# Optimization experiments

Hardware: AMD Instinct MI355X
Metric: run time of the kernel (lower is better)

Reference implementation:

```python
import jax, jax.numpy as jnp
import numpy as np

N = 100000
E = 1600000
D_IN = 64
D_OUT = 64
LN_EPS = 1e-5


def setup_inputs() -> dict:
    key = jax.random.key(0)
    k1, k2, k3 = jax.random.split(key, 3)
    x = jax.random.normal(k1, (N, D_IN), dtype=jnp.float32)
    edge_index = jax.random.randint(k2, (2, E), 0, N, dtype=jnp.int64)
    # nn.Linear(in_dim*2, out_dim): weight [out, 2*in], bias [out]
    W = jax.random.normal(k3, (D_OUT, 2 * D_IN), dtype=jnp.float32) * (1.0 / np.sqrt(2 * D_IN))
    b = jnp.zeros((D_OUT,), dtype=jnp.float32)
    gamma = jnp.ones((D_OUT,), dtype=jnp.float32)
    beta = jnp.zeros((D_OUT,), dtype=jnp.float32)
    return {"x": x, "edge_index": edge_index, "W": W, "b": b, "gamma": gamma, "beta": beta}


def reference(x, edge_index, W, b, gamma, beta):
    i, j = edge_index[0], edge_index[1]          # dst, src
    msg = x[j]                                    # [E, D] gather of source features
    agg = jax.ops.segment_sum(msg, i, num_segments=N)                      # [N, D]
    deg = jax.ops.segment_sum(jnp.ones((E,), x.dtype), i, num_segments=N)  # [N]
    agg = agg / jnp.maximum(deg, 1.0)[:, None]    # mean aggregation
    h = jnp.concatenate([x, agg], axis=-1)        # [N, 2D]
    out = jax.nn.relu(h @ W.T + b)                # [N, D_OUT]
    # LayerNorm over last dim (dropout p=0 -> identity)
    mu = jnp.mean(out, axis=-1, keepdims=True)
    var = jnp.var(out, axis=-1, keepdims=True)
    return (out - mu) * jax.lax.rsqrt(var + LN_EPS) * gamma + beta
```

## Files before the change

kernel.cpp:

```cpp
#include <hip/hip_runtime.h>

#define LN_EPS 1e-5f
#define SBSH   14
#define NSB    7
#define CAP1   268288
#define CPS    131
#define BN     128
#define BC     2368
#define NBK    782
#define CSTRIDE 8

typedef __attribute__((ext_vector_type(8))) short short8;
typedef __attribute__((ext_vector_type(8))) unsigned short ushort8;
typedef __attribute__((ext_vector_type(4))) float v4f;

__device__ __forceinline__ unsigned short f2bf(float f) {
    union { float f; unsigned u; } v; v.f = f;
    unsigned r = (v.u + 0x7fffu + ((v.u >> 16) & 1u)) >> 16;
    return (unsigned short)r;
}
__device__ __forceinline__ float bf2f(unsigned short h) {
    union { unsigned u; float f; } v; v.u = ((unsigned)h) << 16;
    return v.f;
}

__global__ __launch_bounds__(256) void bin1_kernel(
    const int* __restrict__ ei, int* __restrict__ cursor1,
    int* __restrict__ pairs1, const float* __restrict__ W,
    unsigned short* __restrict__ WTB, const float4* __restrict__ x4,
    ushort4* __restrict__ xb4, int E, int N)
{
    __shared__ int h[64];
    __shared__ int hbase[64];
    int t = threadIdx.x;
    int cp = t & 7;

    if (blockIdx.x == 0) {
        for (int i = t; i < 8192; i += 256) {
            int j = i & 7, l = (i >> 3) & 63, st = i >> 9;
            int s = st >> 2, tt = st & 3;
            WTB[i] = f2bf(W[(tt * 16 + (l & 15)) * 128 + s * 32 + (l >> 4) * 8 + j]);
        }
    }
    {
        int total4 = N * 16;
        for (int i = blockIdx.x * 256 + t; i < total4; i += gridDim.x * 256) {
            float4 v = x4[i];
            ushort4 u;
            u.x = f2bf(v.x); u.y = f2bf(v.y); u.z = f2bf(v.z); u.w = f2bf(v.w);
            xb4[i] = u;
        }
    }

    for (int i = t; i < 64; i += 256) h[i] = 0;
    __syncthreads();
    int e0 = blockIdx.x * 4096;
    int dstA[16], srcA[16], rkA[16];
    #pragma unroll
    for (int i = 0; i < 16; ++i) {
        int e = e0 + i * 256 + t;
        int dst = 0, src = 0, rk = -1;
        if (e < E) {
            dst = ei[e]; src = ei[E + e];
            if ((unsigned)dst < (unsigned)N) {
                rk = atomicAdd(&h[cp * 8 + (dst >> SBSH)], 1);
                if ((unsigned)src >= (unsigned)N) src = 0;
            } else { dst = 0; }
        }
        dstA[i] = dst; srcA[i] = src; rkA[i] = rk;
    }
    __syncthreads();
    if (t < 8) {
        int tot = 0;
        #pragma unroll
        for (int c = 0; c < 8; ++c) tot += h[c * 8 + t];
        int gb = tot ? atomicAdd(&cursor1[t * 16], tot) : 0;
        int run = gb;
        #pragma unroll
        for (int c = 0; c < 8; ++c) { hbase[c * 8 + t] = run; run += h[c * 8 + t]; }
    }
    __syncthreads();
    #pragma unroll
    for (int i = 0; i < 16; ++i) {
        if (rkA[i] >= 0) {
            int sb = dstA[i] >> SBSH;
            int slot = hbase[cp * 8 + sb] + rkA[i];
            if (slot < CAP1)
                pairs1[(size_t)sb * CAP1 + slot] = ((dstA[i] & 16383) << 17) | srcA[i];
        }
    }
}

__global__ __launch_bounds__(256) void bin2_kernel(
    const int* __restrict__ cursor1, const int* __restrict__ pairs1,
    int* __restrict__ cursor2, int* __restrict__ pairs2)
{
    __shared__ int h[128], hbase[128];
    int t = threadIdx.x;
    int sb = blockIdx.x / CPS;
    int off0 = (blockIdx.x % CPS) * 2048;
    int tot = cursor1[sb * 16]; if (tot > CAP1) tot = CAP1;
    int m = tot - off0;
    if (m <= 0) return;
    if (m > 2048) m = 2048;
    if (t < 128) h[t] = 0;
    __syncthreads();
    const int* p1 = pairs1 + (size_t)sb * CAP1 + off0;
    int pvA[8], rkA[8];
    #pragma unroll
    for (int i = 0; i < 8; ++i) {
        int idx = i * 256 + t;
        int pv = 0, rk = -1;
        if (idx < m) { pv = p1[idx]; rk = atomicAdd(&h[(pv >> 24) & 127], 1); }
        pvA[i] = pv; rkA[i] = rk;
    }
    __syncthreads();
    if (t < 128) {
        int c = h[t];
        hbase[t] = c ? atomicAdd(&cursor2[(sb * 128 + t) * CSTRIDE], c) : 0;
    }
    __syncthreads();
    #pragma unroll
    for (int i = 0; i < 8; ++i) {
        if (rkA[i] >= 0) {
            int bl = (pvA[i] >> 24) & 127;
            int g = sb * 128 + bl;
            int slot = hbase[bl] + rkA[i];
            if (g < NBK && slot < BC)
                pairs2[(size_t)g * BC + slot] = pvA[i] & 0xFFFFFF;
        }
    }
}

__global__ __launch_bounds__(1024) void sortgather_kernel(
    const int* __restrict__ cursor2, const int* __restrict__ pairs2,
    const unsigned short* __restrict__ xb, unsigned short* __restrict__ aggb, int N)
{
    __shared__ int srcS[BC];
    __shared__ int cnt[BN], off[BN], cur[BN];
    int t = threadIdx.x;
    int g = blockIdx.x;
    int bsize = cursor2[g * CSTRIDE]; if (bsize > BC) bsize = BC;
    const int* pb = pairs2 + (size_t)g * BC;

    if (t < BN) cnt[t] = 0;
    __syncthreads();
    for (int i = t; i < bsize; i += 1024) atomicAdd(&cnt[(pb[i] >> 17) & 127], 1);
    __syncthreads();
    if (t < BN) off[t] = cnt[t];
    __syncthreads();
    for (int s = 1; s < BN; s <<= 1) {
        int v = (t < BN && t >= s) ? off[t - s] : 0;
        __syncthreads();
        if (t < BN) off[t] += v;
        __syncthreads();
    }
    if (t < BN) { int ex = off[t] - cnt[t]; off[t] = ex; cur[t] = ex; }
    __syncthreads();
    for (int i = t; i < bsize; i += 1024) {
        int p = pb[i];
        int pos = atomicAdd(&cur[(p >> 17) & 127], 1);
        srcS[pos] = p & 0x1FFFF;
    }
    __syncthreads();

    int lane = t & 63, wv = t >> 6;
    int g8 = lane >> 3, f8 = lane & 7;
    int ln = wv * 8 + g8;
    int deg = cnt[ln], base = off[ln];

    float acc[8];
    #pragma unroll
    for (int k = 0; k < 8; ++k) acc[k] = 0.f;

    int j = 0;
    for (; j + 2 <= deg; j += 2) {
        int s0 = srcS[base + j];
        int s1 = srcS[base + j + 1];
        short8 a0 = *(const short8*)(xb + (size_t)s0 * 64 + f8 * 8);
        short8 a1 = *(const short8*)(xb + (size_t)s1 * 64 + f8 * 8);
        #pragma unroll
        for (int k = 0; k < 8; ++k) acc[k] += bf2f((unsigned short)a0[k]);
        #pragma unroll
        for (int k = 0; k < 8; ++k) acc[k] += bf2f((unsigned short)a1[k]);
    }
    if (j < deg) {
        int s0 = srcS[base + j];
        short8 a0 = *(const short8*)(xb + (size_t)s0 * 64 + f8 * 8);
        #pragma unroll
        for (int k = 0; k < 8; ++k) acc[k] += bf2f((unsigned short)a0[k]);
    }

    int node = g * BN + ln;
    if (node < N) {
        float inv = 1.0f / fmaxf((float)deg, 1.0f);
        ushort8 r;
        #pragma unroll
        for (int k = 0; k < 8; ++k) r[k] = f2bf(acc[k] * inv);
        *(ushort8*)(aggb + (size_t)node * 64 + f8 * 8) = r;
    }
}

__global__ __launch_bounds__(256) void linear_kernel(
    const unsigned short* __restrict__ xb, const unsigned short* __restrict__ aggb,
    const unsigned short* __restrict__ WTB, const float* __restrict__ b,
    const float* __restrict__ gamma, const float* __restrict__ beta,
    float* __restrict__ out, int N)
{
    int lane = threadIdx.x & 63;
    int wv   = threadIdx.x >> 6;
    int nb   = blockIdx.x * 64 + wv * 16;
    if (nb >= N) return;
    int c = lane & 15, q = lane >> 4;
    int nm = nb + c; if (nm >= N) nm = N - 1;

    short8 bf[4][4];
    const short8* WB = (const short8*)WTB;
    #pragma unroll
    for (int s = 0; s < 4; ++s)
        #pragma unroll
        for (int tt = 0; tt < 4; ++tt)
            bf[s][tt] = WB[(s * 4 + tt) * 64 + lane];

    v4f acc[4];
    #pragma unroll
    for (int tt = 0; tt < 4; ++tt) acc[tt] = 0.f;

    #pragma unroll
    for (int s = 0; s < 2; ++s) {
        short8 af = *(const short8*)(xb + (size_t)nm * 64 + s * 32 + q * 8);
        #pragma unroll
        for (int tt = 0; tt < 4; ++tt)
            acc[tt] = __builtin_amdgcn_mfma_f32_16x16x32_bf16(af, bf[s][tt], acc[tt], 0, 0, 0);
    }
    #pragma unroll
    for (int s = 0; s < 2; ++s) {
        short8 af = *(const short8*)(aggb + (size_t)nm * 64 + s * 32 + q * 8);
        #pragma unroll
        for (int tt = 0; tt < 4; ++tt)
            acc[tt] = __builtin_amdgcn_mfma_f32_16x16x32_bf16(af, bf[2 + s][tt], acc[tt], 0, 0, 0);
    }

    float bb[4], gg[4], be[4];
    #pragma unroll
    for (int tt = 0; tt < 4; ++tt) {
        bb[tt] = b[tt * 16 + c];
        gg[tt] = gamma[tt * 16 + c];
        be[tt] = beta[tt * 16 + c];
    }
    #pragma unroll
    for (int r = 0; r < 4; ++r) {
        int node = nb + q * 4 + r;
        float v[4]; float s0 = 0.f, q0 = 0.f;
        #pragma unroll
        for (int tt = 0; tt < 4; ++tt) {
            float vv = acc[tt][r] + bb[tt];
            vv = fmaxf(vv, 0.f);
            v[tt] = vv; s0 += vv; q0 += vv * vv;
        }
        #pragma unroll
        for (int o = 1; o <= 8; o <<= 1) {
            s0 += __shfl_xor(s0, o);
            q0 += __shfl_xor(q0, o);
        }
        float mu  = s0 * (1.0f / 64.0f);
        float var = q0 * (1.0f / 64.0f) - mu * mu;
        float rs  = rsqrtf(var + LN_EPS);
        if (node < N) {
            #pragma unroll
            for (int tt = 0; tt < 4; ++tt)
                out[(size_t)node * 64 + tt * 16 + c] = (v[tt] - mu) * rs * gg[tt] + be[tt];
        }
    }
}

extern "C" void kernel_launch(void* const* d_in, const int* in_sizes, int n_in,
                              void* d_out, int out_size, void* d_ws, size_t ws_size,
                              hipStream_t stream)
{
    const float* x     = (const float*)d_in[0];
    const int*   ei    = (const int*)d_in[1];
    const float* W     = (const float*)d_in[2];
    const float* b     = (const float*)d_in[3];
    const float* gamma = (const float*)d_in[4];
    const float* beta  = (const float*)d_in[5];

    int N = in_sizes[0] / 64;
    int E = in_sizes[1] / 2;

    int* wsI = (int*)d_ws;
    int* cursor1 = wsI;
    int* cursor2 = wsI + 128;
    unsigned short* WTB = (unsigned short*)(wsI + 128 + 896 * CSTRIDE);
    int* pairs2 = wsI + 128 + 896 * CSTRIDE + 4096;
    unsigned short* xb = (unsigned short*)(pairs2 + (size_t)NBK * BC);

    int* pairs1 = (int*)d_out;
    unsigned short* aggb = (unsigned short*)d_in[1];

    float* out = (float*)d_out;

    hipMemsetAsync(cursor1, 0, (size_t)(128 + 896 * CSTRIDE) * sizeof(int), stream);

    int b1 = (E + 4095) / 4096;
    bin1_kernel<<<b1, 256, 0, stream>>>(ei, cursor1, pairs1, W, WTB,
                                        (const float4*)x, (ushort4*)xb, E, N);

    bin2_kernel<<<NSB * CPS, 256, 0, stream>>>(cursor1, pairs1, cursor2, pairs2);

    sortgather_kernel<<<NBK, 1024, 0, stream>>>(cursor2, pairs2, xb, aggb, N);

    int lb = (N + 63) / 64;
    linear_kernel<<<lb, 256, 0, stream>>>(xb, aggb, WTB, b, gamma, beta, out, N);
}
```

Measured before the change: 172.1 us.

## Gather from feature-sliced bf16 copy of x to improve gather cache locality

The bf16 conversion pass also writes a second copy of x split into four 16-feature slices, each laid out contiguously across nodes. The aggregation kernel then makes four passes, one per slice, with 4-byte per-lane loads, so each pass touches a 3.2 MB working set that fits in cache better than the full 12.8 MB table. The cost is an extra 12.8 MB write in the first kernel, re-reading the source indices four times, and narrower per-lane loads.

Result: slower. 201.5 us (+17.1%).

```diff
diff --git a/kernel.cpp b/kernel.cpp
--- a/kernel.cpp
+++ b/kernel.cpp
@@ -23,12 +23,18 @@
     union { unsigned u; float f; } v; v.u = ((unsigned)h) << 16;
     return v.f;
 }
+__device__ __forceinline__ float bflo(unsigned v) {
+    union { unsigned u; float f; } w; w.u = v << 16; return w.f;
+}
+__device__ __forceinline__ float bfhi(unsigned v) {
+    union { unsigned u; float f; } w; w.u = v & 0xFFFF0000u; return w.f;
+}
 
 __global__ __launch_bounds__(256) void bin1_kernel(
     const int* __restrict__ ei, int* __restrict__ cursor1,
     int* __restrict__ pairs1, const float* __restrict__ W,
     unsigned short* __restrict__ WTB, const float4* __restrict__ x4,
-    ushort4* __restrict__ xb4, int E, int N)
+    ushort4* __restrict__ xb4, ushort4* __restrict__ xs4, int E, int N)
 {
     __shared__ int h[64];
     __shared__ int hbase[64];
@@ -49,6 +55,8 @@
             ushort4 u;
             u.x = f2bf(v.x); u.y = f2bf(v.y); u.z = f2bf(v.z); u.w = f2bf(v.w);
             xb4[i] = u;
+            int node = i >> 4, c = i & 15;
+            xs4[(((c >> 2) * N + node) << 2) + (c & 3)] = u;
         }
     }
 
@@ -134,7 +142,7 @@
 
 __global__ __launch_bounds__(1024) void sortgather_kernel(
     const int* __restrict__ cursor2, const int* __restrict__ pairs2,
-    const unsigned short* __restrict__ xb, unsigned short* __restrict__ aggb, int N)
+    const unsigned short* __restrict__ xs, unsigned short* __restrict__ aggb, int N)
 {
     __shared__ int srcS[BC];
     __shared__ int cnt[BN], off[BN], cur[BN];
@@ -168,36 +176,39 @@
     int g8 = lane >> 3, f8 = lane & 7;
     int ln = wv * 8 + g8;
     int deg = cnt[ln], base = off[ln];
-
-    float acc[8];
-    #pragma unroll
-    for (int k = 0; k < 8; ++k) acc[k] = 0.f;
-
-    int j = 0;
-    for (; j + 2 <= deg; j += 2) {
-        int s0 = srcS[base + j];
-        int s1 = srcS[base + j + 1];
-        short8 a0 = *(const short8*)(xb + (size_t)s0 * 64 + f8 * 8);
-        short8 a1 = *(const short8*)(xb + (size_t)s1 * 64 + f8 * 8);
-        #pragma unroll
-        for (int k = 0; k < 8; ++k) acc[k] += bf2f((unsigned short)a0[k]);
-        #pragma unroll
-        for (int k = 0; k < 8; ++k) acc[k] += bf2f((unsigned short)a1[k]);
-    }
-    if (j < deg) {
-        int s0 = srcS[base + j];
-        short8 a0 = *(const short8*)(xb + (size_t)s0 * 64 + f8 * 8);
-        #pragma unroll
-        for (int k = 0; k < 8; ++k) acc[k] += bf2f((unsigned short)a0[k]);
-    }
-
     int node = g * BN + ln;
-    if (node < N) {
-        float inv = 1.0f / fmaxf((float)deg, 1.0f);
-        ushort8 r;
-        #pragma unroll
-        for (int k = 0; k < 8; ++k) r[k] = f2bf(acc[k] * inv);
-        *(ushort8*)(aggb + (size_t)node * 64 + f8 * 8) = r;
+    float inv = 1.0f / fmaxf((float)deg, 1.0f);
+
+    const unsigned* xs32 = (const unsigned*)xs;
+
+    #pragma unroll
+    for (int p = 0; p < 4; ++p) {
+        size_t pbase = (size_t)p * N * 8;
+        float a0 = 0.f, a1 = 0.f;
+        int j = 0;
+        for (; j + 4 <= deg; j += 4) {
+            int s0 = srcS[base + j];
+            int s1 = srcS[base + j + 1];
+            int s2 = srcS[base + j + 2];
+            int s3 = srcS[base + j + 3];
+            unsigned v0 = xs32[pbase + (size_t)s0 * 8 + f8];
+            unsigned v1 = xs32[pbase + (size_t)s1 * 8 + f8];
+            unsigned v2 = xs32[pbase + (size_t)s2 * 8 + f8];
+            unsigned v3 = xs32[pbase + (size_t)s3 * 8 + f8];
+            a0 += bflo(v0); a1 += bfhi(v0);
+            a0 += bflo(v1); a1 += bfhi(v1);
+            a0 += bflo(v2); a1 += bfhi(v2);
+            a0 += bflo(v3); a1 += bfhi(v3);
+        }
+        for (; j < deg; ++j) {
+            int s0 = srcS[base + j];
+            unsigned v0 = xs32[pbase + (size_t)s0 * 8 + f8];
+            a0 += bflo(v0); a1 += bfhi(v0);
+        }
+        if (node < N) {
+            unsigned pk = (unsigned)f2bf(a0 * inv) | ((unsigned)f2bf(a1 * inv) << 16);
+            *(unsigned*)(aggb + (size_t)node * 64 + p * 16 + f8 * 2) = pk;
+        }
     }
 }
 
@@ -294,6 +305,7 @@
     unsigned short* WTB = (unsigned short*)(wsI + 128 + 896 * CSTRIDE);
     int* pairs2 = wsI + 128 + 896 * CSTRIDE + 4096;
     unsigned short* xb = (unsigned short*)(pairs2 + (size_t)NBK * BC);
+    unsigned short* xs = xb + (size_t)N * 64;
 
     int* pairs1 = (int*)d_out;
     unsigned short* aggb = (unsigned short*)d_in[1];
@@ -304,11 +316,11 @@
 
     int b1 = (E + 4095) / 4096;
     bin1_kernel<<<b1, 256, 0, stream>>>(ei, cursor1, pairs1, W, WTB,
-                                        (const float4*)x, (ushort4*)xb, E, N);
+                                        (const float4*)x, (ushort4*)xb, (ushort4*)xs, E, N);
 
     bin2_kernel<<<NSB * CPS, 256, 0, stream>>>(cursor1, pairs1, cursor2, pairs2);
 
-    sortgather_kernel<<<NBK, 1024, 0, stream>>>(cursor2, pairs2, xb, aggb, N);
+    sortgather_kernel<<<NBK, 1024, 0, stream>>>(cursor2, pairs2, xs, aggb, N);
 
     int lb = (N + 63) / 64;
     linear_kernel<<<lb, 256, 0, stream>>>(xb, aggb, WTB, b, gamma, beta, out, N);
```

## Fuse linear+LayerNorm into sortgather kernel via LDS-staged aggregates

Applied to the files above, without the earlier changes.

Removes the separate linear_kernel launch by keeping each block's 128 aggregated node rows in padded shared memory and running the MFMA linear, ReLU and LayerNorm in the first 8 waves of the same block. This avoids writing aggb to global memory and reading it back, and saves one launch. In exchange, only 8 of the 16 waves do the epilogue, so they run serially after the gather phase. The added LDS buffer may also lower occupancy, and the launch_bounds hint of 8 may push register pressure.

New measurement: 167.5 us. -2.7%, faster.

```diff
diff --git a/kernel.cpp b/kernel.cpp
--- a/kernel.cpp
+++ b/kernel.cpp
@@ -9,6 +9,7 @@
 #define BC     2368
 #define NBK    782
 #define CSTRIDE 8
+#define ASTR   72
 
 typedef __attribute__((ext_vector_type(8))) short short8;
 typedef __attribute__((ext_vector_type(8))) unsigned short ushort8;
@@ -132,12 +133,15 @@
     }
 }
 
-__global__ __launch_bounds__(1024) void sortgather_kernel(
+__global__ __launch_bounds__(1024, 8) void sortgather_kernel(
     const int* __restrict__ cursor2, const int* __restrict__ pairs2,
-    const unsigned short* __restrict__ xb, unsigned short* __restrict__ aggb, int N)
+    const unsigned short* __restrict__ xb, const unsigned short* __restrict__ WTB,
+    const float* __restrict__ b, const float* __restrict__ gamma,
+    const float* __restrict__ beta, float* __restrict__ out, int N)
 {
     __shared__ int srcS[BC];
     __shared__ int cnt[BN], off[BN], cur[BN];
+    __shared__ __align__(16) unsigned short aggS[BN * ASTR];
     int t = threadIdx.x;
     int g = blockIdx.x;
     int bsize = cursor2[g * CSTRIDE]; if (bsize > BC) bsize = BC;
@@ -191,85 +195,73 @@
         for (int k = 0; k < 8; ++k) acc[k] += bf2f((unsigned short)a0[k]);
     }
 
-    int node = g * BN + ln;
-    if (node < N) {
+    {
         float inv = 1.0f / fmaxf((float)deg, 1.0f);
         ushort8 r;
         #pragma unroll
         for (int k = 0; k < 8; ++k) r[k] = f2bf(acc[k] * inv);
-        *(ushort8*)(aggb + (size_t)node * 64 + f8 * 8) = r;
-    }
-}
-
-__global__ __launch_bounds__(256) void linear_kernel(
-    const unsigned short* __restrict__ xb, const unsigned short* __restrict__ aggb,
-    const unsigned short* __restrict__ WTB, const float* __restrict__ b,
-    const float* __restrict__ gamma, const float* __restrict__ beta,
-    float* __restrict__ out, int N)
-{
-    int lane = threadIdx.x & 63;
-    int wv   = threadIdx.x >> 6;
-    int nb   = blockIdx.x * 64 + wv * 16;
-    if (nb >= N) return;
-    int c = lane & 15, q = lane >> 4;
-    int nm = nb + c; if (nm >= N) nm = N - 1;
-
-    short8 bf[4][4];
-    const short8* WB = (const short8*)WTB;
-    #pragma unroll
-    for (int s = 0; s < 4; ++s)
-        #pragma unroll
-        for (int tt = 0; tt < 4; ++tt)
-            bf[s][tt] = WB[(s * 4 + tt) * 64 + lane];
-
-    v4f acc[4];
-    #pragma unroll
-    for (int tt = 0; tt < 4; ++tt) acc[tt] = 0.f;
-
-    #pragma unroll
-    for (int s = 0; s < 2; ++s) {
-        short8 af = *(const short8*)(xb + (size_t)nm * 64 + s * 32 + q * 8);
-        #pragma unroll
-        for (int tt = 0; tt < 4; ++tt)
-            acc[tt] = __builtin_amdgcn_mfma_f32_16x16x32_bf16(af, bf[s][tt], acc[tt], 0, 0, 0);
-    }
-    #pragma unroll
-    for (int s = 0; s < 2; ++s) {
-        short8 af = *(const short8*)(aggb + (size_t)nm * 64 + s * 32 + q * 8);
-        #pragma unroll
-        for (int tt = 0; tt < 4; ++tt)
-            acc[tt] = __builtin_amdgcn_mfma_f32_16x16x32_bf16(af, bf[2 + s][tt], acc[tt], 0, 0, 0);
-    }
-
-    float bb[4], gg[4], be[4];
-    #pragma unroll
-    for (int tt = 0; tt < 4; ++tt) {
-        bb[tt] = b[tt * 16 + c];
-        gg[tt] = gamma[tt * 16 + c];
-        be[tt] = beta[tt * 16 + c];
-    }
-    #pragma unroll
-    for (int r = 0; r < 4; ++r) {
-        int node = nb + q * 4 + r;
-        float v[4]; float s0 = 0.f, q0 = 0.f;
-        #pragma unroll
-        for (int tt = 0; tt < 4; ++tt) {
-            float vv = acc[tt][r] + bb[tt];
-            vv = fmaxf(vv, 0.f);
-            v[tt] = vv; s0 += vv; q0 += vv * vv;
-        }
-        #pragma unroll
-        for (int o = 1; o <= 8; o <<= 1) {
-            s0 += __shfl_xor(s0, o);
-            q0 += __shfl_xor(q0, o);
-        }
-        float mu  = s0 * (1.0f / 64.0f);
-        float var = q0 * (1.0f / 64.0f) - mu * mu;
-        float rs  = rsqrtf(var + LN_EPS);
-        if (node < N) {
+        *(ushort8*)(aggS + ln * ASTR + f8 * 8) = r;
+    }
+    __syncthreads();
+
+    if (wv < 8) {
+        int c = lane & 15, q = lane >> 4;
+        int nb = g * BN + wv * 16;
+        int nm = nb + c; if (nm >= N) nm = N - 1;
+        int lnl = wv * 16 + c;
+
+        const short8* WB = (const short8*)WTB;
+        v4f acc4[4];
+        #pragma unroll
+        for (int tt = 0; tt < 4; ++tt) acc4[tt] = 0.f;
+
+        #pragma unroll
+        for (int s = 0; s < 2; ++s) {
+            short8 af = *(const short8*)(xb + (size_t)nm * 64 + s * 32 + q * 8);
             #pragma unroll
             for (int tt = 0; tt < 4; ++tt)
-                out[(size_t)node * 64 + tt * 16 + c] = (v[tt] - mu) * rs * gg[tt] + be[tt];
+                acc4[tt] = __builtin_amdgcn_mfma_f32_16x16x32_bf16(
+                    af, WB[(s * 4 + tt) * 64 + lane], acc4[tt], 0, 0, 0);
+        }
+        #pragma unroll
+        for (int s = 0; s < 2; ++s) {
+            short8 af = *(const short8*)(aggS + lnl * ASTR + s * 32 + q * 8);
+            #pragma unroll
+            for (int tt = 0; tt < 4; ++tt)
+                acc4[tt] = __builtin_amdgcn_mfma_f32_16x16x32_bf16(
+                    af, WB[((2 + s) * 4 + tt) * 64 + lane], acc4[tt], 0, 0, 0);
+        }
+
+        float bb[4], gg[4], be[4];
+        #pragma unroll
+        for (int tt = 0; tt < 4; ++tt) {
+            bb[tt] = b[tt * 16 + c];
+            gg[tt] = gamma[tt * 16 + c];
+            be[tt] = beta[tt * 16 + c];
+        }
+        #pragma unroll
+        for (int r = 0; r < 4; ++r) {
+            int node = nb + q * 4 + r;
+            float v[4]; float s0 = 0.f, q0 = 0.f;
+            #pragma unroll
+            for (int tt = 0; tt < 4; ++tt) {
+                float vv = acc4[tt][r] + bb[tt];
+                vv = fmaxf(vv, 0.f);
+                v[tt] = vv; s0 += vv; q0 += vv * vv;
+            }
+            #pragma unroll
+            for (int o = 1; o <= 8; o <<= 1) {
+                s0 += __shfl_xor(s0, o);
+                q0 += __shfl_xor(q0, o);
+            }
+            float mu  = s0 * (1.0f / 64.0f);
+            float var = q0 * (1.0f / 64.0f) - mu * mu;
+            float rs  = rsqrtf(var + LN_EPS);
+            if (node < N) {
+                #pragma unroll
+                for (int tt = 0; tt < 4; ++tt)
+                    out[(size_t)node * 64 + tt * 16 + c] = (v[tt] - mu) * rs * gg[tt] + be[tt];
+            }
         }
     }
 }
@@ -296,8 +288,6 @@
     unsigned short* xb = (unsigned short*)(pairs2 + (size_t)NBK * BC);
 
     int* pairs1 = (int*)d_out;
-    unsigned short* aggb = (unsigned short*)d_in[1];
-
     float* out = (float*)d_out;
 
     hipMemsetAsync(cursor1, 0, (size_t)(128 + 896 * CSTRIDE) * sizeof(int), stream);
@@ -308,8 +298,6 @@
 
     bin2_kernel<<<NSB * CPS, 256, 0, stream>>>(cursor1, pairs1, cursor2, pairs2);
 
-    sortgather_kernel<<<NBK, 1024, 0, stream>>>(cursor2, pairs2, xb, aggb, N);
-
-    int lb = (N + 63) / 64;
-    linear_kernel<<<lb, 256, 0, stream>>>(xb, aggb, WTB, b, gamma, beta, out, N);
-}
+    sortgather_kernel<<<NBK, 1024, 0, stream>>>(cursor2, pairs2, xb, WTB,
+                                                b, gamma, beta, out, N);
+}
```
